# Optimization experiments

Hardware: AMD Instinct MI355X
Metric: run time of the kernel (lower is better)

Reference implementation:

```python
import jax, jax.numpy as jnp
import numpy as np

L = 5          # num_layer
EMB = 128      # emb_dim
IN_DIM = 9     # input_dim
EDGE_DIM = 10
N_NODES = 50000
N_EDGES = 600000
N_GRAPHS = 512
BN_EPS = 1e-5


def _bn(x, g, b):
    # training-mode batch norm over axis 0 (biased variance, as torch)
    m = x.mean(axis=0)
    v = x.var(axis=0)
    return (x - m) * jax.lax.rsqrt(v + BN_EPS) * g + b


def setup_inputs() -> dict:
    key = jax.random.key(0)
    ks = jax.random.split(key, 20)
    s = 0.05
    d = {
        'x': jax.random.normal(ks[0], (N_NODES, IN_DIM), jnp.float32),
        'edge_index': jax.random.randint(ks[1], (2, N_EDGES), 0, N_NODES, jnp.int32),
        'edge_attr': jax.random.normal(ks[2], (N_EDGES, EDGE_DIM), jnp.float32),
        'batch': jnp.sort(jax.random.randint(ks[3], (N_NODES,), 0, N_GRAPHS, jnp.int32)),
        'node_W': jax.random.normal(ks[4], (IN_DIM, EMB)) * s,
        'node_b': jnp.zeros((EMB,)),
        'vn_emb': jnp.zeros((1, EMB)),                 # torch init: constant 0
        'eps': jnp.zeros((L,)),                        # GIN eps init 0
        'edge_W': jax.random.normal(ks[5], (L, EDGE_DIM, EMB)) * s,
        'edge_b': jnp.zeros((L, EMB)),
        'conv_W1': jax.random.normal(ks[6], (L, EMB, 2 * EMB)) * s,
        'conv_b1': jnp.zeros((L, 2 * EMB)),
        'conv_bn_g': jnp.ones((L, 2 * EMB)),
        'conv_bn_b': jnp.zeros((L, 2 * EMB)),
        'conv_W2': jax.random.normal(ks[7], (L, 2 * EMB, EMB)) * s,
        'conv_b2': jnp.zeros((L, EMB)),
        'bn_g': jnp.ones((L, EMB)),
        'bn_b': jnp.zeros((L, EMB)),
        'vmlp_W1': jax.random.normal(ks[8], (L - 1, EMB, 2 * EMB)) * s,
        'vmlp_b1': jnp.zeros((L - 1, 2 * EMB)),
        'vmlp_bn1_g': jnp.ones((L - 1, 2 * EMB)),
        'vmlp_bn1_b': jnp.zeros((L - 1, 2 * EMB)),
        'vmlp_W2': jax.random.normal(ks[9], (L - 1, 2 * EMB, EMB)) * s,
        'vmlp_b2': jnp.zeros((L - 1, EMB)),
        'vmlp_bn2_g': jnp.ones((L - 1, EMB)),
        'vmlp_bn2_b': jnp.zeros((L - 1, EMB)),
    }
    return d


def reference(x, edge_index, edge_attr, batch,
              node_W, node_b, vn_emb, eps, edge_W, edge_b,
              conv_W1, conv_b1, conv_bn_g, conv_bn_b, conv_W2, conv_b2,
              bn_g, bn_b,
              vmlp_W1, vmlp_b1, vmlp_bn1_g, vmlp_bn1_b,
              vmlp_W2, vmlp_b2, vmlp_bn2_g, vmlp_bn2_b):
    n = x.shape[0]
    src, dst = edge_index[0], edge_index[1]
    vn = jnp.broadcast_to(vn_emb[0], (N_GRAPHS, EMB))  # virtual node per graph
    h = x @ node_W + node_b                            # node encoder
    for l in range(L):
        h_in = h + vn[batch]                           # broadcast virtual node
        # DrugGINConv
        e = edge_attr @ edge_W[l] + edge_b[l]          # edge encoder [E,EMB]
        msg = jax.nn.relu(h_in[src] + e)               # gather + message
        agg = jax.ops.segment_sum(msg, dst, num_segments=n)  # scatter-add
        t = (1.0 + eps[l]) * h_in + agg
        t = _bn(t @ conv_W1[l] + conv_b1[l], conv_bn_g[l], conv_bn_b[l])
        t = jax.nn.relu(t) @ conv_W2[l] + conv_b2[l]
        t = _bn(t, bn_g[l], bn_b[l])                   # outer batch norm
        h = t if l == L - 1 else jax.nn.relu(t)        # dropout identity (p=0)
        if l < L - 1:
            vtmp = jax.ops.segment_sum(h_in, batch, num_segments=N_GRAPHS) + vn
            u = _bn(vtmp @ vmlp_W1[l] + vmlp_b1[l], vmlp_bn1_g[l], vmlp_bn1_b[l])
            u = jax.nn.relu(u) @ vmlp_W2[l] + vmlp_b2[l]
            vn = jax.nn.relu(_bn(u, vmlp_bn2_g[l], vmlp_bn2_b[l]))
    return h
```

## Files before the change

kernel.cpp:

```cpp
#include <hip/hip_runtime.h>


#define EMB 128
#define NGR 512
#define NLAYER 5
static constexpr float BN_EPS = 1e-5f;

typedef __attribute__((ext_vector_type(8))) short short8v;
typedef __attribute__((ext_vector_type(4))) float f32x4;

__device__ __forceinline__ ushort f2bf(float f) {
  union { float f; unsigned u; } c; c.f = f;
  return (ushort)((c.u + 0x7FFFu + ((c.u >> 16) & 1u)) >> 16);
}
__device__ __forceinline__ float bf2f(ushort h) {
  union { unsigned u; float f; } c; c.u = ((unsigned)h) << 16;
  return c.f;
}


__global__ void init_kernel(int* __restrict__ deg, int ndeg,
                            float* __restrict__ stats, int nstats,
                            float* __restrict__ vn, const float* __restrict__ vn_emb) {
  int idx = blockIdx.x * blockDim.x + threadIdx.x;
  if (idx < ndeg) deg[idx] = 0;
  if (idx < nstats) stats[idx] = 0.f;
  if (idx < NGR * EMB) vn[idx] = vn_emb[idx & (EMB - 1)];
}

__global__ void deg_kernel(const int* __restrict__ ei, int* __restrict__ deg, int E) {
  int e = blockIdx.x * blockDim.x + threadIdx.x;
  if (e < E) atomicAdd(&deg[ei[E + e]], 1);
}


__global__ void scan1_kernel(const int* __restrict__ deg, int* __restrict__ bsum, int n) {
  __shared__ int ws[4];
  int t = threadIdx.x;
  int base = blockIdx.x * 2048 + t * 8;
  int s = 0;
  #pragma unroll
  for (int i = 0; i < 8; ++i) {
    int idx = base + i;
    if (idx < n) s += deg[idx];
  }
  #pragma unroll
  for (int off = 32; off; off >>= 1) s += __shfl_down(s, off);
  if ((t & 63) == 0) ws[t >> 6] = s;
  __syncthreads();
  if (t == 0) bsum[blockIdx.x] = ws[0] + ws[1] + ws[2] + ws[3];
}

__global__ void scan2_kernel(const int* __restrict__ bsum, int* __restrict__ boff,
                             int* __restrict__ row_n, int nb) {
  int t = threadIdx.x;
  int mine = (t < nb) ? bsum[t] : 0;
  int v = mine;
  #pragma unroll
  for (int off = 1; off < 64; off <<= 1) {
    int u = __shfl_up(v, off);
    if (t >= off) v += u;
  }
  if (t < nb) boff[t] = v - mine;
  if (t == nb - 1) *row_n = v;
}

__global__ __launch_bounds__(256) void scan3_kernel(const int* __restrict__ deg,
                                                    const int* __restrict__ boff,
                                                    int* __restrict__ row_start,
                                                    int* __restrict__ cursor, int n) {
  __shared__ int lsum[256];
  int t = threadIdx.x;
  int base = blockIdx.x * 2048 + t * 8;
  int loc[8];
  int s = 0;
  #pragma unroll
  for (int i = 0; i < 8; ++i) {
    int idx = base + i;
    int d = (idx < n) ? deg[idx] : 0;
    loc[i] = s;
    s += d;
  }
  lsum[t] = s;
  __syncthreads();
  #pragma unroll
  for (int off = 1; off < 256; off <<= 1) {
    int v2 = (t >= off) ? lsum[t - off] : 0;
    __syncthreads();
    lsum[t] += v2;
    __syncthreads();
  }
  int toff = boff[blockIdx.x] + lsum[t] - s;
  #pragma unroll
  for (int i = 0; i < 8; ++i) {
    int idx = base + i;
    if (idx < n) {
      int rs = toff + loc[i];
      row_start[idx] = rs;
      cursor[idx] = rs;
    }
  }
}

__global__ void fill_kernel(const int* __restrict__ ei, int* __restrict__ cursor,
                            int2* __restrict__ el, int E) {
  int e = blockIdx.x * blockDim.x + threadIdx.x;
  if (e < E) {
    int d = ei[E + e];
    int pos = atomicAdd(&cursor[d], 1);
    el[pos] = make_int2(e, ei[e]);
  }
}

__global__ void bounds_kernel(const int* __restrict__ batch, int* __restrict__ gstart,
                              int n, int ng) {
  int g = blockIdx.x * blockDim.x + threadIdx.x;
  if (g > ng) return;
  int lo = 0, hi = n;
  while (lo < hi) {
    int mid = (lo + hi) >> 1;
    if (batch[mid] < g) lo = mid + 1; else hi = mid;
  }
  gstart[g] = lo;
}

__global__ void wtrans_kernel(const float* __restrict__ W, ushort* __restrict__ Wth,
                              ushort* __restrict__ Wtl, int K, int N, int total) {
  int idx = blockIdx.x * blockDim.x + threadIdx.x;
  if (idx >= total) return;
  int kk = idx % K;
  int t = idx / K;
  int nn = t % N;
  int l = t / N;
  float v = W[((size_t)l * K + kk) * N + nn];
  ushort h = f2bf(v);
  Wth[idx] = h;
  Wtl[idx] = f2bf(v - bf2f(h));
}

__global__ void encoder_kernel(const float* __restrict__ x, const float* __restrict__ W,
                               const float* __restrict__ b, float* __restrict__ h0, int n) {
  __shared__ float Ws[9][EMB];
  __shared__ float bs[EMB];
  int t = threadIdx.x;
  if (t < EMB) {
    #pragma unroll
    for (int k = 0; k < 9; ++k) Ws[k][t] = W[k * EMB + t];
    bs[t] = b[t];
  }
  __syncthreads();
  int total = n * EMB;
  for (int idx = blockIdx.x * blockDim.x + t; idx < total; idx += gridDim.x * blockDim.x) {
    int i = idx >> 7, j = idx & 127;
    const float* xr = x + i * 9;
    float acc = bs[j];
    #pragma unroll
    for (int k = 0; k < 9; ++k) acc = fmaf(xr[k], Ws[k][j], acc);
    h0[idx] = acc;
  }
}


template <bool RAW>
__global__ void hin_kernel(const float* __restrict__ src, const float* __restrict__ vn,
                           const int* __restrict__ batch, const float* __restrict__ s2raw,
                           const float* __restrict__ g2, const float* __restrict__ b2,
                           float* __restrict__ h_in, int n) {
  __shared__ float sc[EMB], sh[EMB];
  if (!RAW) {
    int j = threadIdx.x;
    if (j < EMB) {
      float s = s2raw[j], q = s2raw[EMB + j];
      float mean = s / (float)n;
      float var = q / (float)n - mean * mean;
      float scl = g2[j] * rsqrtf(var + BN_EPS);
      sc[j] = scl;
      sh[j] = b2[j] - mean * scl;
    }
    __syncthreads();
  }
  int total = n * EMB;
  for (int idx = blockIdx.x * blockDim.x + threadIdx.x; idx < total; idx += gridDim.x * blockDim.x) {
    int i = idx >> 7, j = idx & 127;
    float v = src[idx];
    if (!RAW) v = fmaxf(fmaf(v, sc[j], sh[j]), 0.f);
    h_in[idx] = v + vn[batch[i] * EMB + j];
  }
}

__global__ void out_kernel(const float* __restrict__ t2, const float* __restrict__ s2raw,
                           const float* __restrict__ g2, const float* __restrict__ b2,
                           float* __restrict__ out, int n) {
  __shared__ float sc[EMB], sh[EMB];
  int j0 = threadIdx.x;
  if (j0 < EMB) {
    float s = s2raw[j0], q = s2raw[EMB + j0];
    float mean = s / (float)n;
    float var = q / (float)n - mean * mean;
    float scl = g2[j0] * rsqrtf(var + BN_EPS);
    sc[j0] = scl;
    sh[j0] = b2[j0] - mean * scl;
  }
  __syncthreads();
  int total = n * EMB;
  for (int idx = blockIdx.x * blockDim.x + threadIdx.x; idx < total; idx += gridDim.x * blockDim.x) {
    int j = idx & 127;
    out[idx] = fmaf(t2[idx], sc[j], sh[j]);
  }
}

__global__ void vnsum_kernel(const float* __restrict__ h_in, const int* __restrict__ gstart,
                             const float* __restrict__ vn, float* __restrict__ vnsum) {
  int g = blockIdx.x;
  int j = threadIdx.x;
  int s0 = gstart[g], s1 = gstart[g + 1];
  float acc = vn[g * EMB + j];
  for (int i = s0; i < s1; ++i) acc += h_in[i * EMB + j];
  vnsum[g * EMB + j] = acc;
}

__global__ void agg_kernel(const float* __restrict__ h_in, const int* __restrict__ row_start,
                           const int2* __restrict__ el,
                           const float* __restrict__ edge_attr, const float* __restrict__ eW,
                           const float* __restrict__ eb, const float* __restrict__ eps_p, int l,
                           float* __restrict__ t_pre, int n) {
  __shared__ float W[10][EMB];
  __shared__ float bia[EMB];
  int j = threadIdx.x;
  #pragma unroll
  for (int k = 0; k < 10; ++k) W[k][j] = eW[k * EMB + j];
  bia[j] = eb[j];
  float epsv = 1.f + eps_p[l];
  __syncthreads();
  for (int i = blockIdx.x; i < n; i += gridDim.x) {
    int s0 = row_start[i], s1 = row_start[i + 1];
    float acc = epsv * h_in[(size_t)i * EMB + j];
    int p = s0;
    for (; p + 4 <= s1; p += 4) {
      int2 e0 = el[p], e1 = el[p + 1], e2 = el[p + 2], e3 = el[p + 3];
      float hv0 = h_in[(size_t)e0.y * EMB + j];
      float hv1 = h_in[(size_t)e1.y * EMB + j];
      float hv2 = h_in[(size_t)e2.y * EMB + j];
      float hv3 = h_in[(size_t)e3.y * EMB + j];
      const float* ea0 = edge_attr + (size_t)e0.x * 10;
      const float* ea1 = edge_attr + (size_t)e1.x * 10;
      const float* ea2 = edge_attr + (size_t)e2.x * 10;
      const float* ea3 = edge_attr + (size_t)e3.x * 10;
      float v0 = bia[j], v1 = bia[j], v2 = bia[j], v3 = bia[j];
      #pragma unroll
      for (int k = 0; k < 10; ++k) {
        float w = W[k][j];
        v0 = fmaf(ea0[k], w, v0);
        v1 = fmaf(ea1[k], w, v1);
        v2 = fmaf(ea2[k], w, v2);
        v3 = fmaf(ea3[k], w, v3);
      }
      acc += fmaxf(v0 + hv0, 0.f) + fmaxf(v1 + hv1, 0.f) +
             fmaxf(v2 + hv2, 0.f) + fmaxf(v3 + hv3, 0.f);
    }
    for (; p < s1; ++p) {
      int2 e0 = el[p];
      float hv0 = h_in[(size_t)e0.y * EMB + j];
      const float* ea0 = edge_attr + (size_t)e0.x * 10;
      float v0 = bia[j];
      #pragma unroll
      for (int k = 0; k < 10; ++k) v0 = fmaf(ea0[k], W[k][j], v0);
      acc += fmaxf(v0 + hv0, 0.f);
    }
    t_pre[(size_t)i * EMB + j] = acc;
  }
}

template <int KT, int NT, bool BN_A, bool STATS>
__global__ __launch_bounds__(256) void gemm_mfma(
    const float* __restrict__ A, const ushort* __restrict__ Bth,
    const ushort* __restrict__ Btl, const float* __restrict__ bias,
    float* __restrict__ C, int M,
    const float* __restrict__ bnraw, const float* __restrict__ bng,
    const float* __restrict__ bnb, float* __restrict__ statraw) {
  constexpr int BM = 128, BN = 128, BK = 32;
  constexpr int LDK = BK + 8;
  constexpr int KSTEPS = KT / BK;
  __shared__ ushort Ah[BM][LDK], Al[BM][LDK];
  __shared__ ushort Bh[BN][LDK], Bl[BN][LDK];
  __shared__ float red[8][BN], redq[8][BN];
  constexpr int SCN = BN_A ? KT : 1;
  __shared__ float scS[SCN], shS[SCN];

  int tid = threadIdx.x;
  if (BN_A) {
    for (int k = tid; k < KT; k += 256) {
      float s = bnraw[k], q = bnraw[KT + k];
      float mean = s / (float)M;
      float var = q / (float)M - mean * mean;
      float scl = bng[k] * rsqrtf(var + BN_EPS);
      scS[k] = scl;
      shS[k] = bnb[k] - mean * scl;
    }
  }

  int wv = tid >> 6, lane = tid & 63;
  int wr = wv >> 1, wc = wv & 1;
  int lr = lane & 15, kg = lane >> 4;
  int bm0 = blockIdx.x * BM;
  int gc0 = blockIdx.y * BN;

  int sr = tid >> 1;
  int skq = (tid & 1) * 16;

  f32x4 acc[4][4];
  #pragma unroll
  for (int fm = 0; fm < 4; ++fm)
    #pragma unroll
    for (int fn = 0; fn < 4; ++fn) {
      float b = bias[gc0 + wc * 64 + fn * 16 + lr];
      acc[fm][fn][0] = b; acc[fm][fn][1] = b; acc[fm][fn][2] = b; acc[fm][fn][3] = b;
    }

  for (int kt = 0; kt < KSTEPS; ++kt) {
    __syncthreads();
    {
      int grow = bm0 + sr;
      const float* ap = A + (size_t)grow * KT + kt * BK + skq;
      short8v ah0, al0, ah1, al1;
      #pragma unroll
      for (int u = 0; u < 4; ++u) {
        float4 v = (grow < M) ? *reinterpret_cast<const float4*>(ap + u * 4)
                              : make_float4(0.f, 0.f, 0.f, 0.f);
        if (BN_A) {
          int gk = kt * BK + skq + u * 4;
          v.x = fmaxf(fmaf(v.x, scS[gk + 0], shS[gk + 0]), 0.f);
          v.y = fmaxf(fmaf(v.y, scS[gk + 1], shS[gk + 1]), 0.f);
          v.z = fmaxf(fmaf(v.z, scS[gk + 2], shS[gk + 2]), 0.f);
          v.w = fmaxf(fmaf(v.w, scS[gk + 3], shS[gk + 3]), 0.f);
        }
        float vv0 = v.x, vv1 = v.y, vv2 = v.z, vv3 = v.w;
        ushort h0 = f2bf(vv0), h1 = f2bf(vv1), h2 = f2bf(vv2), h3 = f2bf(vv3);
        ushort w0 = f2bf(vv0 - bf2f(h0)), w1 = f2bf(vv1 - bf2f(h1));
        ushort w2 = f2bf(vv2 - bf2f(h2)), w3 = f2bf(vv3 - bf2f(h3));
        if (u < 2) {
          ah0[u * 4 + 0] = (short)h0; ah0[u * 4 + 1] = (short)h1;
          ah0[u * 4 + 2] = (short)h2; ah0[u * 4 + 3] = (short)h3;
          al0[u * 4 + 0] = (short)w0; al0[u * 4 + 1] = (short)w1;
          al0[u * 4 + 2] = (short)w2; al0[u * 4 + 3] = (short)w3;
        } else {
          ah1[(u - 2) * 4 + 0] = (short)h0; ah1[(u - 2) * 4 + 1] = (short)h1;
          ah1[(u - 2) * 4 + 2] = (short)h2; ah1[(u - 2) * 4 + 3] = (short)h3;
          al1[(u - 2) * 4 + 0] = (short)w0; al1[(u - 2) * 4 + 1] = (short)w1;
          al1[(u - 2) * 4 + 2] = (short)w2; al1[(u - 2) * 4 + 3] = (short)w3;
        }
      }
      *(short8v*)&Ah[sr][skq] = ah0;
      *(short8v*)&Ah[sr][skq + 8] = ah1;
      *(short8v*)&Al[sr][skq] = al0;
      *(short8v*)&Al[sr][skq + 8] = al1;
    }
    {
      const ushort* bph = Bth + (size_t)(gc0 + sr) * KT + kt * BK + skq;
      const ushort* bpl = Btl + (size_t)(gc0 + sr) * KT + kt * BK + skq;
      *(short8v*)&Bh[sr][skq] = *(const short8v*)bph;
      *(short8v*)&Bh[sr][skq + 8] = *(const short8v*)(bph + 8);
      *(short8v*)&Bl[sr][skq] = *(const short8v*)bpl;
      *(short8v*)&Bl[sr][skq + 8] = *(const short8v*)(bpl + 8);
    }
    __syncthreads();
    short8v a_h[4], a_l[4], b_h[4], b_l[4];
    #pragma unroll
    for (int f = 0; f < 4; ++f) {
      a_h[f] = *(const short8v*)&Ah[wr * 64 + f * 16 + lr][kg * 8];
      a_l[f] = *(const short8v*)&Al[wr * 64 + f * 16 + lr][kg * 8];
      b_h[f] = *(const short8v*)&Bh[wc * 64 + f * 16 + lr][kg * 8];
      b_l[f] = *(const short8v*)&Bl[wc * 64 + f * 16 + lr][kg * 8];
    }
    #pragma unroll
    for (int fm = 0; fm < 4; ++fm)
      #pragma unroll
      for (int fn = 0; fn < 4; ++fn) {
        acc[fm][fn] = __builtin_amdgcn_mfma_f32_16x16x32_bf16(a_h[fm], b_h[fn], acc[fm][fn], 0, 0, 0);
        acc[fm][fn] = __builtin_amdgcn_mfma_f32_16x16x32_bf16(a_h[fm], b_l[fn], acc[fm][fn], 0, 0, 0);
        acc[fm][fn] = __builtin_amdgcn_mfma_f32_16x16x32_bf16(a_l[fm], b_h[fn], acc[fm][fn], 0, 0, 0);
      }
  }

  #pragma unroll
  for (int fm = 0; fm < 4; ++fm) {
    int rb = bm0 + wr * 64 + fm * 16 + kg * 4;
    #pragma unroll
    for (int i = 0; i < 4; ++i) {
      int grow = rb + i;
      if (grow < M) {
        float* cp = C + (size_t)grow * NT + gc0 + wc * 64 + lr;
        #pragma unroll
        for (int fn = 0; fn < 4; ++fn) cp[fn * 16] = acc[fm][fn][i];
      }
    }
  }

  if (STATS) {
    #pragma unroll
    for (int fn = 0; fn < 4; ++fn) {
      float s = 0.f, q = 0.f;
      #pragma unroll
      for (int fm = 0; fm < 4; ++fm) {
        int rb = bm0 + wr * 64 + fm * 16 + kg * 4;
        #pragma unroll
        for (int i = 0; i < 4; ++i) {
          if (rb + i < M) {
            float v = acc[fm][fn][i];
            s += v;
            q = fmaf(v, v, q);
          }
        }
      }
      red[wr * 4 + kg][wc * 64 + fn * 16 + lr] = s;
      redq[wr * 4 + kg][wc * 64 + fn * 16 + lr] = q;
    }
    __syncthreads();
    if (tid < BN) {
      float s = 0.f, q = 0.f;
      #pragma unroll
      for (int r2 = 0; r2 < 8; ++r2) {
        s += red[r2][tid];
        q += redq[r2][tid];
      }
      int gcol = gc0 + tid;
      atomicAdd(&statraw[gcol], s);
      atomicAdd(&statraw[NT + gcol], q);
    }
  }
}


__global__ void vmlp1_kernel(const float* __restrict__ vtmp, const float* __restrict__ W,
                             const float* __restrict__ b, float* __restrict__ u1,
                             float* __restrict__ vs1raw) {
  __shared__ float a[EMB];
  int g = blockIdx.x;
  int j = threadIdx.x;
  if (j < EMB) a[j] = vtmp[g * EMB + j];
  __syncthreads();
  float acc = b[j];
  #pragma unroll 8
  for (int k = 0; k < EMB; ++k) acc = fmaf(a[k], W[k * 256 + j], acc);
  u1[g * 256 + j] = acc;
  atomicAdd(&vs1raw[j], acc);
  atomicAdd(&vs1raw[256 + j], acc * acc);
}

__global__ void vmlp2_kernel(const float* __restrict__ u1, const float* __restrict__ vs1raw,
                             const float* __restrict__ g1, const float* __restrict__ b1,
                             const float* __restrict__ W, const float* __restrict__ b2,
                             float* __restrict__ u2, float* __restrict__ vs2raw) {
  __shared__ float a[256];
  __shared__ float sc[256], sh[256];
  int g = blockIdx.x;
  int j = threadIdx.x;
  for (int k = j; k < 256; k += EMB) {
    float s = vs1raw[k], q = vs1raw[256 + k];
    float mean = s / (float)NGR;
    float var = q / (float)NGR - mean * mean;
    float scl = g1[k] * rsqrtf(var + BN_EPS);
    sc[k] = scl;
    sh[k] = b1[k] - mean * scl;
  }
  __syncthreads();
  for (int k = j; k < 256; k += EMB)
    a[k] = fmaxf(fmaf(u1[g * 256 + k], sc[k], sh[k]), 0.f);
  __syncthreads();
  float acc = b2[j];
  #pragma unroll 8
  for (int k = 0; k < 256; ++k) acc = fmaf(a[k], W[k * EMB + j], acc);
  u2[g * EMB + j] = acc;
  atomicAdd(&vs2raw[j], acc);
  atomicAdd(&vs2raw[EMB + j], acc * acc);
}

__global__ void vnupd_kernel(const float* __restrict__ u2, const float* __restrict__ vs2raw,
                             const float* __restrict__ g2, const float* __restrict__ b2,
                             float* __restrict__ vn) {
  __shared__ float sc[EMB], sh[EMB];
  int g = blockIdx.x;
  int j = threadIdx.x;
  {
    float s = vs2raw[j], q = vs2raw[EMB + j];
    float mean = s / (float)NGR;
    float var = q / (float)NGR - mean * mean;
    float scl = g2[j] * rsqrtf(var + BN_EPS);
    sc[j] = scl;
    sh[j] = b2[j] - mean * scl;
  }
  __syncthreads();
  vn[g * EMB + j] = fmaxf(fmaf(u2[g * EMB + j], sc[j], sh[j]), 0.f);
}


extern "C" void kernel_launch(void* const* d_in, const int* in_sizes, int n_in,
                              void* d_out, int out_size, void* d_ws, size_t ws_size,
                              hipStream_t stream) {
  const float* x        = (const float*)d_in[0];
  const int*   ei       = (const int*)d_in[1];
  const float* eattr    = (const float*)d_in[2];
  const int*   batch    = (const int*)d_in[3];
  const float* node_W   = (const float*)d_in[4];
  const float* node_b   = (const float*)d_in[5];
  const float* vn_emb   = (const float*)d_in[6];
  const float* eps      = (const float*)d_in[7];
  const float* edge_W   = (const float*)d_in[8];
  const float* edge_b   = (const float*)d_in[9];
  const float* conv_W1  = (const float*)d_in[10];
  const float* conv_b1  = (const float*)d_in[11];
  const float* cbn_g    = (const float*)d_in[12];
  const float* cbn_b    = (const float*)d_in[13];
  const float* conv_W2  = (const float*)d_in[14];
  const float* conv_b2  = (const float*)d_in[15];
  const float* bn_g     = (const float*)d_in[16];
  const float* bn_b     = (const float*)d_in[17];
  const float* vW1      = (const float*)d_in[18];
  const float* vb1      = (const float*)d_in[19];
  const float* vbn1_g   = (const float*)d_in[20];
  const float* vbn1_b   = (const float*)d_in[21];
  const float* vW2      = (const float*)d_in[22];
  const float* vb2      = (const float*)d_in[23];
  const float* vbn2_g   = (const float*)d_in[24];
  const float* vbn2_b   = (const float*)d_in[25];

  const int n = in_sizes[0] / 9;
  const int E = in_sizes[1] / 2;
  const int nb = (n + 2047) / 2048;

  char* p = (char*)d_ws;
  auto carve = [&](size_t bytes) {
    char* r = p;
    p += (bytes + 255) & ~(size_t)255;
    return r;
  };
  float* tpre   = (float*)carve((size_t)n * EMB * 4);
  float* h_in   = (float*)carve((size_t)n * EMB * 4);
  float* t1     = (float*)carve((size_t)n * 256 * 4);
  float* t2     = (float*)carve((size_t)n * EMB * 4);
  float* vn     = (float*)carve((size_t)NGR * EMB * 4);
  float* vnsum  = (float*)carve((size_t)NGR * EMB * 4);
  float* u1     = (float*)carve((size_t)NGR * 256 * 4);
  float* u2     = (float*)carve((size_t)NGR * EMB * 4);
  float* stats  = (float*)carve((size_t)NLAYER * 1536 * 4);
  int* deg      = (int*)carve((size_t)n * 4);
  int* rstart   = (int*)carve((size_t)(n + 1) * 4);
  int* cursor   = (int*)carve((size_t)n * 4);
  int2* el      = (int2*)carve((size_t)E * 8);
  int* gstart   = (int*)carve((size_t)(NGR + 1) * 4);
  int* bsum     = (int*)carve((size_t)64 * 4);
  int* boff     = (int*)carve((size_t)64 * 4);
  ushort* wt1h  = (ushort*)carve((size_t)NLAYER * 256 * 128 * 2);
  ushort* wt1l  = (ushort*)carve((size_t)NLAYER * 256 * 128 * 2);
  ushort* wt2h  = (ushort*)carve((size_t)NLAYER * 128 * 256 * 2);
  ushort* wt2l  = (ushort*)carve((size_t)NLAYER * 128 * 256 * 2);
  float* h0     = tpre;

  auto s1  = [&](int l) { return stats + (size_t)l * 1536; };
  auto s2  = [&](int l) { return stats + (size_t)l * 1536 + 512; };
  auto vs1 = [&](int l) { return stats + (size_t)l * 1536 + 768; };
  auto vs2 = [&](int l) { return stats + (size_t)l * 1536 + 1280; };

  init_kernel<<<(NGR * EMB + 255) / 256, 256, 0, stream>>>(deg, n, stats, NLAYER * 1536, vn, vn_emb);
  deg_kernel<<<(E + 255) / 256, 256, 0, stream>>>(ei, deg, E);
  scan1_kernel<<<nb, 256, 0, stream>>>(deg, bsum, n);
  scan2_kernel<<<1, 64, 0, stream>>>(bsum, boff, rstart + n, nb);
  scan3_kernel<<<nb, 256, 0, stream>>>(deg, boff, rstart, cursor, n);
  fill_kernel<<<(E + 255) / 256, 256, 0, stream>>>(ei, cursor, el, E);
  bounds_kernel<<<(NGR + 1 + 255) / 256, 256, 0, stream>>>(batch, gstart, n, NGR);
  {
    int tot1 = NLAYER * 128 * 256;
    wtrans_kernel<<<(tot1 + 255) / 256, 256, 0, stream>>>(conv_W1, wt1h, wt1l, 128, 256, tot1);
    int tot2 = NLAYER * 256 * 128;
    wtrans_kernel<<<(tot2 + 255) / 256, 256, 0, stream>>>(conv_W2, wt2h, wt2l, 256, 128, tot2);
  }
  encoder_kernel<<<2048, 256, 0, stream>>>(x, node_W, node_b, h0, n);

  const int mtiles = (n + 127) / 128;

  for (int l = 0; l < NLAYER; ++l) {
    if (l == 0)
      hin_kernel<true><<<4096, 256, 0, stream>>>(h0, vn, batch, nullptr, nullptr, nullptr, h_in, n);
    else
      hin_kernel<false><<<4096, 256, 0, stream>>>(t2, vn, batch, s2(l - 1),
                                                  bn_g + (size_t)(l - 1) * EMB,
                                                  bn_b + (size_t)(l - 1) * EMB, h_in, n);
    if (l < NLAYER - 1)
      vnsum_kernel<<<NGR, EMB, 0, stream>>>(h_in, gstart, vn, vnsum);

    agg_kernel<<<n, EMB, 0, stream>>>(h_in, rstart, el, eattr,
                                      edge_W + (size_t)l * 10 * EMB,
                                      edge_b + (size_t)l * EMB, eps, l, tpre, n);

    gemm_mfma<128, 256, false, true><<<dim3(mtiles, 2), 256, 0, stream>>>(
        tpre, wt1h + (size_t)l * 256 * 128, wt1l + (size_t)l * 256 * 128,
        conv_b1 + (size_t)l * 256, t1, n, nullptr, nullptr, nullptr, s1(l));

    gemm_mfma<256, 128, true, true><<<dim3(mtiles, 1), 256, 0, stream>>>(
        t1, wt2h + (size_t)l * 128 * 256, wt2l + (size_t)l * 128 * 256,
        conv_b2 + (size_t)l * 128, t2, n,
        s1(l), cbn_g + (size_t)l * 256, cbn_b + (size_t)l * 256, s2(l));

    if (l < NLAYER - 1) {
      vmlp1_kernel<<<NGR, 256, 0, stream>>>(vnsum, vW1 + (size_t)l * 128 * 256,
                                            vb1 + (size_t)l * 256, u1, vs1(l));
      vmlp2_kernel<<<NGR, EMB, 0, stream>>>(u1, vs1(l), vbn1_g + (size_t)l * 256,
                                            vbn1_b + (size_t)l * 256,
                                            vW2 + (size_t)l * 256 * 128,
                                            vb2 + (size_t)l * EMB, u2, vs2(l));
      vnupd_kernel<<<NGR, EMB, 0, stream>>>(u2, vs2(l), vbn2_g + (size_t)l * EMB,
                                            vbn2_b + (size_t)l * EMB, vn);
    }
  }

  out_kernel<<<4096, 256, 0, stream>>>(t2, s2(NLAYER - 1),
                                       bn_g + (size_t)(NLAYER - 1) * EMB,
                                       bn_b + (size_t)(NLAYER - 1) * EMB,
                                       (float*)d_out, n);
}
```

Before: 1.265 ms.

## Gather neighbor features in bf16 and emit pre-split bf16 hi/lo GEMM input

The hin kernel now also writes a bf16 copy of h_in, and the aggregation kernel gathers neighbor rows from it, halving gather bytes for the random-access edge loop. The aggregation kernel writes its output directly as bf16 hi/lo pairs, so the first GEMM loads pre-split operands instead of converting fp32 in its tile loader. The grid-stride loop is replaced by one node per block. Rounding neighbor features to bf16 before the message add reduces precision relative to the fp32 reference, and hin does an extra store.

```diff
diff --git a/kernel.cpp b/kernel.cpp
--- a/kernel.cpp
+++ b/kernel.cpp
@@ -165,7 +165,7 @@
 __global__ void hin_kernel(const float* __restrict__ src, const float* __restrict__ vn,
                            const int* __restrict__ batch, const float* __restrict__ s2raw,
                            const float* __restrict__ g2, const float* __restrict__ b2,
-                           float* __restrict__ h_in, int n) {
+                           float* __restrict__ h_in, ushort* __restrict__ h16, int n) {
   __shared__ float sc[EMB], sh[EMB];
   if (!RAW) {
     int j = threadIdx.x;
@@ -184,7 +184,9 @@
     int i = idx >> 7, j = idx & 127;
     float v = src[idx];
     if (!RAW) v = fmaxf(fmaf(v, sc[j], sh[j]), 0.f);
-    h_in[idx] = v + vn[batch[i] * EMB + j];
+    float hv = v + vn[batch[i] * EMB + j];
+    h_in[idx] = hv;
+    h16[idx] = f2bf(hv);
   }
 }
 
@@ -219,11 +221,12 @@
   vnsum[g * EMB + j] = acc;
 }
 
-__global__ void agg_kernel(const float* __restrict__ h_in, const int* __restrict__ row_start,
-                           const int2* __restrict__ el,
-                           const float* __restrict__ edge_attr, const float* __restrict__ eW,
-                           const float* __restrict__ eb, const float* __restrict__ eps_p, int l,
-                           float* __restrict__ t_pre, int n) {
+__global__ __launch_bounds__(128) void agg_kernel(
+    const float* __restrict__ h_in, const ushort* __restrict__ h16,
+    const int* __restrict__ row_start, const int2* __restrict__ el,
+    const float* __restrict__ edge_attr, const float* __restrict__ eW,
+    const float* __restrict__ eb, const float* __restrict__ eps_p, int l,
+    ushort* __restrict__ tpre_h, ushort* __restrict__ tpre_l, int n) {
   __shared__ float W[10][EMB];
   __shared__ float bia[EMB];
   int j = threadIdx.x;
@@ -232,49 +235,53 @@
   bia[j] = eb[j];
   float epsv = 1.f + eps_p[l];
   __syncthreads();
-  for (int i = blockIdx.x; i < n; i += gridDim.x) {
-    int s0 = row_start[i], s1 = row_start[i + 1];
-    float acc = epsv * h_in[(size_t)i * EMB + j];
-    int p = s0;
-    for (; p + 4 <= s1; p += 4) {
-      int2 e0 = el[p], e1 = el[p + 1], e2 = el[p + 2], e3 = el[p + 3];
-      float hv0 = h_in[(size_t)e0.y * EMB + j];
-      float hv1 = h_in[(size_t)e1.y * EMB + j];
-      float hv2 = h_in[(size_t)e2.y * EMB + j];
-      float hv3 = h_in[(size_t)e3.y * EMB + j];
-      const float* ea0 = edge_attr + (size_t)e0.x * 10;
-      const float* ea1 = edge_attr + (size_t)e1.x * 10;
-      const float* ea2 = edge_attr + (size_t)e2.x * 10;
-      const float* ea3 = edge_attr + (size_t)e3.x * 10;
-      float v0 = bia[j], v1 = bia[j], v2 = bia[j], v3 = bia[j];
-      #pragma unroll
-      for (int k = 0; k < 10; ++k) {
-        float w = W[k][j];
-        v0 = fmaf(ea0[k], w, v0);
-        v1 = fmaf(ea1[k], w, v1);
-        v2 = fmaf(ea2[k], w, v2);
-        v3 = fmaf(ea3[k], w, v3);
-      }
-      acc += fmaxf(v0 + hv0, 0.f) + fmaxf(v1 + hv1, 0.f) +
-             fmaxf(v2 + hv2, 0.f) + fmaxf(v3 + hv3, 0.f);
-    }
-    for (; p < s1; ++p) {
-      int2 e0 = el[p];
-      float hv0 = h_in[(size_t)e0.y * EMB + j];
-      const float* ea0 = edge_attr + (size_t)e0.x * 10;
-      float v0 = bia[j];
-      #pragma unroll
-      for (int k = 0; k < 10; ++k) v0 = fmaf(ea0[k], W[k][j], v0);
-      acc += fmaxf(v0 + hv0, 0.f);
-    }
-    t_pre[(size_t)i * EMB + j] = acc;
-  }
-}
-
-template <int KT, int NT, bool BN_A, bool STATS>
+
+  int i = blockIdx.x;
+  int s0 = row_start[i], s1 = row_start[i + 1];
+  float acc = epsv * h_in[(size_t)i * EMB + j];
+  int p = s0;
+  for (; p + 4 <= s1; p += 4) {
+    int2 e0 = el[p], e1 = el[p + 1], e2 = el[p + 2], e3 = el[p + 3];
+    float hv0 = bf2f(h16[(size_t)e0.y * EMB + j]);
+    float hv1 = bf2f(h16[(size_t)e1.y * EMB + j]);
+    float hv2 = bf2f(h16[(size_t)e2.y * EMB + j]);
+    float hv3 = bf2f(h16[(size_t)e3.y * EMB + j]);
+    const float* ea0 = edge_attr + (size_t)e0.x * 10;
+    const float* ea1 = edge_attr + (size_t)e1.x * 10;
+    const float* ea2 = edge_attr + (size_t)e2.x * 10;
+    const float* ea3 = edge_attr + (size_t)e3.x * 10;
+    float v0 = bia[j], v1 = bia[j], v2 = bia[j], v3 = bia[j];
+    #pragma unroll
+    for (int k = 0; k < 10; ++k) {
+      float w = W[k][j];
+      v0 = fmaf(ea0[k], w, v0);
+      v1 = fmaf(ea1[k], w, v1);
+      v2 = fmaf(ea2[k], w, v2);
+      v3 = fmaf(ea3[k], w, v3);
+    }
+    acc += fmaxf(v0 + hv0, 0.f) + fmaxf(v1 + hv1, 0.f) +
+           fmaxf(v2 + hv2, 0.f) + fmaxf(v3 + hv3, 0.f);
+  }
+  for (; p < s1; ++p) {
+    int2 e0 = el[p];
+    float hv0 = bf2f(h16[(size_t)e0.y * EMB + j]);
+    const float* ea0 = edge_attr + (size_t)e0.x * 10;
+    float v0 = bia[j];
+    #pragma unroll
+    for (int k = 0; k < 10; ++k) v0 = fmaf(ea0[k], W[k][j], v0);
+    acc += fmaxf(v0 + hv0, 0.f);
+  }
+  ushort hh = f2bf(acc);
+  tpre_h[(size_t)i * EMB + j] = hh;
+  tpre_l[(size_t)i * EMB + j] = f2bf(acc - bf2f(hh));
+}
+
+template <int KT, int NT, bool BN_A, bool STATS, bool APRE>
 __global__ __launch_bounds__(256) void gemm_mfma(
-    const float* __restrict__ A, const ushort* __restrict__ Bth,
-    const ushort* __restrict__ Btl, const float* __restrict__ bias,
+    const float* __restrict__ A, const ushort* __restrict__ Ath,
+    const ushort* __restrict__ Atl,
+    const ushort* __restrict__ Bth, const ushort* __restrict__ Btl,
+    const float* __restrict__ bias,
     float* __restrict__ C, int M,
     const float* __restrict__ bnraw, const float* __restrict__ bng,
     const float* __restrict__ bnb, float* __restrict__ statraw) {
@@ -321,39 +328,58 @@
     __syncthreads();
     {
       int grow = bm0 + sr;
-      const float* ap = A + (size_t)grow * KT + kt * BK + skq;
-      short8v ah0, al0, ah1, al1;
-      #pragma unroll
-      for (int u = 0; u < 4; ++u) {
-        float4 v = (grow < M) ? *reinterpret_cast<const float4*>(ap + u * 4)
-                              : make_float4(0.f, 0.f, 0.f, 0.f);
-        if (BN_A) {
-          int gk = kt * BK + skq + u * 4;
-          v.x = fmaxf(fmaf(v.x, scS[gk + 0], shS[gk + 0]), 0.f);
-          v.y = fmaxf(fmaf(v.y, scS[gk + 1], shS[gk + 1]), 0.f);
-          v.z = fmaxf(fmaf(v.z, scS[gk + 2], shS[gk + 2]), 0.f);
-          v.w = fmaxf(fmaf(v.w, scS[gk + 3], shS[gk + 3]), 0.f);
+      if (APRE) {
+        short8v z;
+        #pragma unroll
+        for (int q2 = 0; q2 < 8; ++q2) z[q2] = 0;
+        if (grow < M) {
+          const ushort* aph = Ath + (size_t)grow * KT + kt * BK + skq;
+          const ushort* apl = Atl + (size_t)grow * KT + kt * BK + skq;
+          *(short8v*)&Ah[sr][skq] = *(const short8v*)aph;
+          *(short8v*)&Ah[sr][skq + 8] = *(const short8v*)(aph + 8);
+          *(short8v*)&Al[sr][skq] = *(const short8v*)apl;
+          *(short8v*)&Al[sr][skq + 8] = *(const short8v*)(apl + 8);
+        } else {
+          *(short8v*)&Ah[sr][skq] = z;
+          *(short8v*)&Ah[sr][skq + 8] = z;
+          *(short8v*)&Al[sr][skq] = z;
+          *(short8v*)&Al[sr][skq + 8] = z;
         }
-        float vv0 = v.x, vv1 = v.y, vv2 = v.z, vv3 = v.w;
-        ushort h0 = f2bf(vv0), h1 = f2bf(vv1), h2 = f2bf(vv2), h3 = f2bf(vv3);
-        ushort w0 = f2bf(vv0 - bf2f(h0)), w1 = f2bf(vv1 - bf2f(h1));
-        ushort w2 = f2bf(vv2 - bf2f(h2)), w3 = f2bf(vv3 - bf2f(h3));
-        if (u < 2) {
-          ah0[u * 4 + 0] = (short)h0; ah0[u * 4 + 1] = (short)h1;
-          ah0[u * 4 + 2] = (short)h2; ah0[u * 4 + 3] = (short)h3;
-          al0[u * 4 + 0] = (short)w0; al0[u * 4 + 1] = (short)w1;
-          al0[u * 4 + 2] = (short)w2; al0[u * 4 + 3] = (short)w3;
-        } else {
-          ah1[(u - 2) * 4 + 0] = (short)h0; ah1[(u - 2) * 4 + 1] = (short)h1;
-          ah1[(u - 2) * 4 + 2] = (short)h2; ah1[(u - 2) * 4 + 3] = (short)h3;
-          al1[(u - 2) * 4 + 0] = (short)w0; al1[(u - 2) * 4 + 1] = (short)w1;
-          al1[(u - 2) * 4 + 2] = (short)w2; al1[(u - 2) * 4 + 3] = (short)w3;
+      } else {
+        const float* ap = A + (size_t)grow * KT + kt * BK + skq;
+        short8v ah0, al0, ah1, al1;
+        #pragma unroll
+        for (int u = 0; u < 4; ++u) {
+          float4 v = (grow < M) ? *reinterpret_cast<const float4*>(ap + u * 4)
+                                : make_float4(0.f, 0.f, 0.f, 0.f);
+          if (BN_A) {
+            int gk = kt * BK + skq + u * 4;
+            v.x = fmaxf(fmaf(v.x, scS[gk + 0], shS[gk + 0]), 0.f);
+            v.y = fmaxf(fmaf(v.y, scS[gk + 1], shS[gk + 1]), 0.f);
+            v.z = fmaxf(fmaf(v.z, scS[gk + 2], shS[gk + 2]), 0.f);
+            v.w = fmaxf(fmaf(v.w, scS[gk + 3], shS[gk + 3]), 0.f);
+          }
+          float vv0 = v.x, vv1 = v.y, vv2 = v.z, vv3 = v.w;
+          ushort h0 = f2bf(vv0), h1 = f2bf(vv1), h2 = f2bf(vv2), h3 = f2bf(vv3);
+          ushort w0 = f2bf(vv0 - bf2f(h0)), w1 = f2bf(vv1 - bf2f(h1));
+          ushort w2 = f2bf(vv2 - bf2f(h2)), w3 = f2bf(vv3 - bf2f(h3));
+          if (u < 2) {
+            ah0[u * 4 + 0] = (short)h0; ah0[u * 4 + 1] = (short)h1;
+            ah0[u * 4 + 2] = (short)h2; ah0[u * 4 + 3] = (short)h3;
+            al0[u * 4 + 0] = (short)w0; al0[u * 4 + 1] = (short)w1;
+            al0[u * 4 + 2] = (short)w2; al0[u * 4 + 3] = (short)w3;
+          } else {
+            ah1[(u - 2) * 4 + 0] = (short)h0; ah1[(u - 2) * 4 + 1] = (short)h1;
+            ah1[(u - 2) * 4 + 2] = (short)h2; ah1[(u - 2) * 4 + 3] = (short)h3;
+            al1[(u - 2) * 4 + 0] = (short)w0; al1[(u - 2) * 4 + 1] = (short)w1;
+            al1[(u - 2) * 4 + 2] = (short)w2; al1[(u - 2) * 4 + 3] = (short)w3;
+          }
         }
+        *(short8v*)&Ah[sr][skq] = ah0;
+        *(short8v*)&Ah[sr][skq + 8] = ah1;
+        *(short8v*)&Al[sr][skq] = al0;
+        *(short8v*)&Al[sr][skq + 8] = al1;
       }
-      *(short8v*)&Ah[sr][skq] = ah0;
-      *(short8v*)&Ah[sr][skq + 8] = ah1;
-      *(short8v*)&Al[sr][skq] = al0;
-      *(short8v*)&Al[sr][skq + 8] = al1;
     }
     {
       const ushort* bph = Bth + (size_t)(gc0 + sr) * KT + kt * BK + skq;
@@ -534,10 +560,12 @@
     p += (bytes + 255) & ~(size_t)255;
     return r;
   };
-  float* tpre   = (float*)carve((size_t)n * EMB * 4);
   float* h_in   = (float*)carve((size_t)n * EMB * 4);
+  ushort* h16   = (ushort*)carve((size_t)n * EMB * 2);
   float* t1     = (float*)carve((size_t)n * 256 * 4);
   float* t2     = (float*)carve((size_t)n * EMB * 4);
+  ushort* tpre_h = (ushort*)carve((size_t)n * EMB * 2);
+  ushort* tpre_l = (ushort*)carve((size_t)n * EMB * 2);
   float* vn     = (float*)carve((size_t)NGR * EMB * 4);
   float* vnsum  = (float*)carve((size_t)NGR * EMB * 4);
   float* u1     = (float*)carve((size_t)NGR * 256 * 4);
@@ -554,7 +582,7 @@
   ushort* wt1l  = (ushort*)carve((size_t)NLAYER * 256 * 128 * 2);
   ushort* wt2h  = (ushort*)carve((size_t)NLAYER * 128 * 256 * 2);
   ushort* wt2l  = (ushort*)carve((size_t)NLAYER * 128 * 256 * 2);
-  float* h0     = tpre;
+  float* h0     = t1;
 
   auto s1  = [&](int l) { return stats + (size_t)l * 1536; };
   auto s2  = [&](int l) { return stats + (size_t)l * 1536 + 512; };
@@ -580,24 +608,25 @@
 
   for (int l = 0; l < NLAYER; ++l) {
     if (l == 0)
-      hin_kernel<true><<<4096, 256, 0, stream>>>(h0, vn, batch, nullptr, nullptr, nullptr, h_in, n);
+      hin_kernel<true><<<4096, 256, 0, stream>>>(h0, vn, batch, nullptr, nullptr, nullptr,
+                                                 h_in, h16, n);
     else
       hin_kernel<false><<<4096, 256, 0, stream>>>(t2, vn, batch, s2(l - 1),
                                                   bn_g + (size_t)(l - 1) * EMB,
-                                                  bn_b + (size_t)(l - 1) * EMB, h_in, n);
+                                                  bn_b + (size_t)(l - 1) * EMB, h_in, h16, n);
     if (l < NLAYER - 1)
       vnsum_kernel<<<NGR, EMB, 0, stream>>>(h_in, gstart, vn, vnsum);
 
-    agg_kernel<<<n, EMB, 0, stream>>>(h_in, rstart, el, eattr,
+    agg_kernel<<<n, EMB, 0, stream>>>(h_in, h16, rstart, el, eattr,
                                       edge_W + (size_t)l * 10 * EMB,
-                                      edge_b + (size_t)l * EMB, eps, l, tpre, n);
-
-    gemm_mfma<128, 256, false, true><<<dim3(mtiles, 2), 256, 0, stream>>>(
-        tpre, wt1h + (size_t)l * 256 * 128, wt1l + (size_t)l * 256 * 128,
+                                      edge_b + (size_t)l * EMB, eps, l, tpre_h, tpre_l, n);
+
+    gemm_mfma<128, 256, false, true, true><<<dim3(mtiles, 2), 256, 0, stream>>>(
+        nullptr, tpre_h, tpre_l, wt1h + (size_t)l * 256 * 128, wt1l + (size_t)l * 256 * 128,
         conv_b1 + (size_t)l * 256, t1, n, nullptr, nullptr, nullptr, s1(l));
 
-    gemm_mfma<256, 128, true, true><<<dim3(mtiles, 1), 256, 0, stream>>>(
-        t1, wt2h + (size_t)l * 128 * 256, wt2l + (size_t)l * 128 * 256,
+    gemm_mfma<256, 128, true, true, false><<<dim3(mtiles, 1), 256, 0, stream>>>(
+        t1, nullptr, nullptr, wt2h + (size_t)l * 128 * 256, wt2l + (size_t)l * 128 * 256,
         conv_b2 + (size_t)l * 128, t2, n,
         s1(l), cbn_g + (size_t)l * 256, cbn_b + (size_t)l * 256, s2(l));
 
```

Result: no change. 1.280 ms (+1.2%).
